# Kernel tuning notes

Measured on AMD Instinct MI355X. Metric: run time of the kernel, lower is better.

Reference implementation:

```python
import jax, jax.numpy as jnp
import numpy as np

S = 4096            # num tokens (single causal sequence)
HID = 1024          # hidden_size
NH = 16             # num query heads
NKV = 4             # num kv heads
HD = 64             # head_dim
THETA = 10000.0
Q_SIZE = NH * HD
KV_SIZE = NKV * HD


def setup_inputs() -> dict:
    key = jax.random.key(0)
    k1, k2, k3 = jax.random.split(key, 3)
    return {
        "positions": jnp.arange(S, dtype=jnp.int32),
        "hidden_states": jax.random.normal(k1, (S, 2 * HID), dtype=jnp.float32),
        "w_qkv": jax.random.normal(k2, (Q_SIZE + 2 * KV_SIZE, 2 * HID), dtype=jnp.float32) * 0.02,
        "w_o": jax.random.normal(k3, (HID, Q_SIZE), dtype=jnp.float32) * 0.02,
    }


def _rope(x, positions):
    # x: [S, H, HD]; neox-style rotate-half RoPE
    half = HD // 2
    inv_freq = 1.0 / (THETA ** (jnp.arange(0, half, dtype=jnp.float32) / half))
    freqs = positions.astype(jnp.float32)[:, None] * inv_freq  # [S, half]
    cos = jnp.cos(freqs)[:, None, :]  # [S, 1, half]
    sin = jnp.sin(freqs)[:, None, :]
    x1, x2 = x[..., :half], x[..., half:]
    return jnp.concatenate([x1 * cos - x2 * sin, x2 * cos + x1 * sin], axis=-1)


def reference(positions, hidden_states, w_qkv, w_o):
    qkv = hidden_states @ w_qkv.T  # [S, Q_SIZE + 2*KV_SIZE]
    q = qkv[:, :Q_SIZE].reshape(S, NH, HD)
    k = qkv[:, Q_SIZE:Q_SIZE + KV_SIZE].reshape(S, NKV, HD)
    v = qkv[:, Q_SIZE + KV_SIZE:].reshape(S, NKV, HD)
    q = _rope(q, positions)
    k = _rope(k, positions)
    # GQA: group query heads over kv heads
    g = NH // NKV
    qg = q.reshape(S, NKV, g, HD)
    scale = HD ** -0.5
    scores = jnp.einsum("qhgd,thd->hgqt", qg, k) * scale  # [NKV, g, S, S]
    causal = positions[:, None] >= positions[None, :]      # [S, S]
    scores = jnp.where(causal[None, None], scores, jnp.finfo(scores.dtype).min)
    probs = jax.nn.softmax(scores, axis=-1)
    o = jnp.einsum("hgqt,thd->qhgd", probs, v).reshape(S, Q_SIZE)
    return o @ w_o.T  # [S, HID]
```

## Files before the change

### kernel.cpp

```cpp
#include <hip/hip_runtime.h>
#include <math.h>

#define S_LEN   4096
#define NHEADS  16
#define NKVH    4
#define HDIM    64
#define QKV_N   1536
#define HID2    2048
#define OUT_N   1024

typedef __attribute__((ext_vector_type(8))) __bf16 bf16x8;
typedef __attribute__((ext_vector_type(4))) __bf16 bf16x4;
typedef __attribute__((ext_vector_type(4))) float  f32x4;

#define GL_LDS16(gaddr, laddr)                                                  \
  __builtin_amdgcn_global_load_lds(                                             \
      (const __attribute__((address_space(1))) unsigned int*)(gaddr),           \
      (__attribute__((address_space(3))) unsigned int*)(laddr), 16, 0, 0)

__global__ __launch_bounds__(256) void cvt_all(const float* __restrict__ hid,
                                               const float* __restrict__ wq,
                                               const float* __restrict__ wo,
                                               __bf16* __restrict__ hid_bf,
                                               __bf16* __restrict__ wq_bf,
                                               __bf16* __restrict__ wo_bf) {
  const int n1 = S_LEN * HID2;
  const int n2 = QKV_N * HID2;
  int i = (blockIdx.x * blockDim.x + threadIdx.x) * 8;
  const float* src; __bf16* dst; int off;
  if (i < n1)           { src = hid; dst = hid_bf; off = i; }
  else if (i < n1 + n2) { src = wq;  dst = wq_bf;  off = i - n1; }
  else                  { src = wo;  dst = wo_bf;  off = i - n1 - n2; }
  float4 a = *(const float4*)(src + off);
  float4 b = *(const float4*)(src + off + 4);
  bf16x8 o = {(__bf16)a.x,(__bf16)a.y,(__bf16)a.z,(__bf16)a.w,
              (__bf16)b.x,(__bf16)b.y,(__bf16)b.z,(__bf16)b.w};
  *(bf16x8*)(dst + off) = o;
}

__global__ __launch_bounds__(256) void rope_table(const int* __restrict__ positions,
                                                  float* __restrict__ ct,
                                                  float* __restrict__ st) {
  int i = blockIdx.x * blockDim.x + threadIdx.x;
  int s = i >> 5, d = i & 31;
  double inv = pow(10000.0, -(double)d / 32.0);
  double fr = (double)positions[s] * inv;
  ct[i] = (float)cos(fr);
  st[i] = (float)sin(fr);
}

template<int BM, bool C_BF16>
__global__ __launch_bounds__(256) void gemm_m97(const __bf16* __restrict__ A,
                                                const __bf16* __restrict__ B,
                                                void* __restrict__ Cp,
                                                int M, int N, int K) {
  constexpr int TM = BM / 32;
  __shared__ __align__(16) __bf16 As[BM * 32];
  __shared__ __align__(16) __bf16 Bs[128 * 32];
  const int tid  = threadIdx.x;
  const int bm   = blockIdx.x, bn = blockIdx.y;
  const int wave = tid >> 6, lane = tid & 63;
  const int quad = lane >> 4, col = lane & 15;
  const int wm = (wave >> 1) * (BM / 2), wn = (wave & 1) * 64;

  const int lrow = lane >> 2, lcol = (lane & 3) * 8;
  const __bf16* Ag = A + (size_t)(bm * BM + wave * (BM / 4) + lrow) * K + lcol;
  const __bf16* Bg = B + (size_t)(bn * 128 + wave * 32 + lrow) * K + lcol;
  __bf16* AsW = As + wave * (BM / 4) * 32;
  __bf16* BsW = Bs + wave * 32 * 32;

  f32x4 acc[TM][4];
#pragma unroll
  for (int i = 0; i < TM; ++i)
#pragma unroll
    for (int j = 0; j < 4; ++j) acc[i][j] = (f32x4){0.f, 0.f, 0.f, 0.f};

  for (int kk = 0; kk < K; kk += 32) {
    __syncthreads();
#pragma unroll
    for (int u = 0; u < BM / 64; ++u)
      GL_LDS16(Ag + kk + (size_t)(u * 16) * K, AsW + u * 16 * 32);
    GL_LDS16(Bg + kk,                  BsW);
    GL_LDS16(Bg + kk + (size_t)16 * K, BsW + 16 * 32);
    __syncthreads();

    bf16x8 a[TM], b[4];
#pragma unroll
    for (int tm = 0; tm < TM; ++tm)
      a[tm] = *(const bf16x8*)&As[(wm + tm * 16 + col) * 32 + quad * 8];
#pragma unroll
    for (int tn = 0; tn < 4; ++tn)
      b[tn] = *(const bf16x8*)&Bs[(wn + tn * 16 + col) * 32 + quad * 8];
#pragma unroll
    for (int tm = 0; tm < TM; ++tm)
#pragma unroll
      for (int tn = 0; tn < 4; ++tn)
        acc[tm][tn] = __builtin_amdgcn_mfma_f32_16x16x32_bf16(a[tm], b[tn], acc[tm][tn], 0, 0, 0);
  }

#pragma unroll
  for (int tm = 0; tm < TM; ++tm)
#pragma unroll
    for (int tn = 0; tn < 4; ++tn) {
      int row = bm * BM + wm + tm * 16 + quad * 4;
      int cg  = bn * 128 + wn + tn * 16 + col;
#pragma unroll
      for (int r = 0; r < 4; ++r) {
        if constexpr (C_BF16)
          ((__bf16*)Cp)[(size_t)(row + r) * N + cg] = (__bf16)acc[tm][tn][r];
        else
          ((float*)Cp)[(size_t)(row + r) * N + cg] = acc[tm][tn][r];
      }
    }
}

__global__ __launch_bounds__(256) void rope_cast(const __bf16* __restrict__ qkv,
                                                 const float* __restrict__ ct,
                                                 const float* __restrict__ st,
                                                 __bf16* __restrict__ qb,
                                                 __bf16* __restrict__ kb) {
  int g = blockIdx.x * blockDim.x + threadIdx.x;
  int d = g & 31;
  int rem = g >> 5;
  int head = rem % 20;
  int s = rem / 20;
  bool isq = head < NHEADS;
  const __bf16* src = qkv + (size_t)s * QKV_N + (isq ? head * 64 : 1024 + (head - 16) * 64);
  float c  = ct[s * 32 + d];
  float sn = st[s * 32 + d];
  float x1 = (float)src[d], x2 = (float)src[d + 32];
  float y1 = x1 * c - x2 * sn;
  float y2 = x2 * c + x1 * sn;
  float scl = isq ? 0.125f : 1.0f;
  __bf16* dst = isq ? (qb + (size_t)s * 1024 + head * 64)
                    : (kb + (size_t)s * 256 + (head - 16) * 64);
  dst[d]      = (__bf16)(y1 * scl);
  dst[d + 32] = (__bf16)(y2 * scl);
}

__global__ __launch_bounds__(256) void v_transpose(const __bf16* __restrict__ qkv,
                                                   __bf16* __restrict__ vT) {
  __shared__ __align__(16) __bf16 Ts[64][72];
  const int sb = blockIdx.x, kvh = blockIdx.y, t = threadIdx.x;
  const int r = t >> 2, c16 = (t & 3) * 16;
  const __bf16* src = qkv + (size_t)(sb * 64 + r) * QKV_N + 1280 + kvh * 64 + c16;
  bf16x8 v0 = *(const bf16x8*)src;
  bf16x8 v1 = *(const bf16x8*)(src + 8);
#pragma unroll
  for (int u = 0; u < 8; ++u) {
    Ts[c16 + u][r]     = v0[u];
    Ts[c16 + 8 + u][r] = v1[u];
  }
  __syncthreads();
  __bf16* dst = vT + ((size_t)kvh * 64 + r) * S_LEN + sb * 64 + c16;
  *(bf16x8*)dst       = *(const bf16x8*)&Ts[r][c16];
  *(bf16x8*)(dst + 8) = *(const bf16x8*)&Ts[r][c16 + 8];
}

__global__ __launch_bounds__(256) void attn_mfma2(const __bf16* __restrict__ qg,
                                                  const __bf16* __restrict__ kg,
                                                  const __bf16* __restrict__ vg,
                                                  __bf16* __restrict__ ob) {
  __shared__ __align__(16) __bf16 lds[26624];
  __bf16* Qs = lds;
  __bf16* Ks = lds + 8192;
  __bf16* Vs = lds + 17408;

  const int tid = threadIdx.x;
  const int h = blockIdx.x;
  const int yy = blockIdx.y;
  const int qb = (yy < 16) ? yy : 47 - yy;
  const int kvh = h >> 2;
  const int wave = tid >> 6, lane = tid & 63;
  const int quad = lane >> 4, col = lane & 15;
  const int quad4 = quad * 4;
  const int qbase = qb * 128 + wave * 32;
  const int ntiles = 2 * qb + 2;

  {
    const int r = tid >> 1, c = (tid & 1) * 32;
    const __bf16* src = qg + (size_t)(qb * 128 + r) * 1024 + h * 64 + c;
    *(bf16x8*)&Qs[r * 64 + c]      = *(const bf16x8*)(src);
    *(bf16x8*)&Qs[r * 64 + c + 8]  = *(const bf16x8*)(src + 8);
    *(bf16x8*)&Qs[r * 64 + c + 16] = *(const bf16x8*)(src + 16);
    *(bf16x8*)&Qs[r * 64 + c + 24] = *(const bf16x8*)(src + 24);
  }

  const int sr = tid >> 2, sc = (tid & 3) * 16;
  const __bf16* kptr = kg + (size_t)sr * 256 + kvh * 64 + sc;
  const __bf16* vptr = vg + ((size_t)kvh * 64 + sr) * S_LEN + sc;
  bf16x8 kr0 = *(const bf16x8*)(kptr);
  bf16x8 kr1 = *(const bf16x8*)(kptr + 8);
  bf16x8 vr0 = *(const bf16x8*)(vptr);
  bf16x8 vr1 = *(const bf16x8*)(vptr + 8);

  __syncthreads();

  bf16x8 qf[2][2];
#pragma unroll
  for (int nq = 0; nq < 2; ++nq)
#pragma unroll
    for (int ks = 0; ks < 2; ++ks)
      qf[nq][ks] = *(const bf16x8*)&Qs[(wave * 32 + nq * 16 + col) * 64 + ks * 32 + quad * 8];

  __bf16* Pw = Qs + wave * 2048;

  f32x4 o[2][4];
  float lacc[2] = {0.f, 0.f};
#pragma unroll
  for (int i = 0; i < 2; ++i)
#pragma unroll
    for (int j = 0; j < 4; ++j) o[i][j] = (f32x4){0.f, 0.f, 0.f, 0.f};

  for (int kt = 0; kt < ntiles; ++kt) {
    const int cur = kt & 1;
    {
      __bf16* kd = Ks + cur * 4608 + sr * 72 + sc;
      *(bf16x8*)kd       = kr0;
      *(bf16x8*)(kd + 8) = kr1;
      __bf16* vd = Vs + cur * 4608 + sr * 72 + sc;
      *(bf16x8*)vd       = vr0;
      *(bf16x8*)(vd + 8) = vr1;
    }
    if (kt + 1 < ntiles) {
      const __bf16* kn = kptr + (size_t)(kt + 1) * 64 * 256;
      const __bf16* vn = vptr + (size_t)(kt + 1) * 64;
      kr0 = *(const bf16x8*)(kn);
      kr1 = *(const bf16x8*)(kn + 8);
      vr0 = *(const bf16x8*)(vn);
      vr1 = *(const bf16x8*)(vn + 8);
    }
    __syncthreads();

    if (kt * 64 > qbase + 31) continue;

    f32x4 sf[4][2];
#pragma unroll
    for (int mt = 0; mt < 4; ++mt)
#pragma unroll
      for (int nq = 0; nq < 2; ++nq) sf[mt][nq] = (f32x4){0.f, 0.f, 0.f, 0.f};
#pragma unroll
    for (int ks = 0; ks < 2; ++ks) {
      bf16x8 kf[4];
#pragma unroll
      for (int mt = 0; mt < 4; ++mt)
        kf[mt] = *(const bf16x8*)&Ks[cur * 4608 + (mt * 16 + col) * 72 + ks * 32 + quad * 8];
#pragma unroll
      for (int mt = 0; mt < 4; ++mt)
#pragma unroll
        for (int nq = 0; nq < 2; ++nq)
          sf[mt][nq] = __builtin_amdgcn_mfma_f32_16x16x32_bf16(kf[mt], qf[nq][ks], sf[mt][nq], 0, 0, 0);
    }

    const bool full = (kt * 64 + 63 <= qbase);
#pragma unroll
    for (int mt = 0; mt < 4; ++mt) {
      const int tb = mt * 16 + quad4;
#pragma unroll
      for (int nq = 0; nq < 2; ++nq) {
        const int thr = qbase + nq * 16 + col - kt * 64;
        float p0 = __expf(sf[mt][nq][0]);
        float p1 = __expf(sf[mt][nq][1]);
        float p2 = __expf(sf[mt][nq][2]);
        float p3 = __expf(sf[mt][nq][3]);
        if (!full) {
          if (tb + 0 > thr) p0 = 0.f;
          if (tb + 1 > thr) p1 = 0.f;
          if (tb + 2 > thr) p2 = 0.f;
          if (tb + 3 > thr) p3 = 0.f;
        }
        lacc[nq] += (p0 + p1) + (p2 + p3);
        const int g = ((mt * 2 + (quad >> 1)) ^ (col & 7));
        bf16x4 pk = {(__bf16)p0, (__bf16)p1, (__bf16)p2, (__bf16)p3};
        *(bf16x4*)&Pw[(nq * 16 + col) * 64 + g * 8 + (quad & 1) * 4] = pk;
      }
    }

#pragma unroll
    for (int ks = 0; ks < 2; ++ks) {
      bf16x8 pf[2], vf[4];
#pragma unroll
      for (int mq = 0; mq < 2; ++mq)
        pf[mq] = *(const bf16x8*)&Pw[(mq * 16 + col) * 64 + (((ks * 4 + quad) ^ (col & 7)) * 8)];
#pragma unroll
      for (int nd = 0; nd < 4; ++nd)
        vf[nd] = *(const bf16x8*)&Vs[cur * 4608 + (nd * 16 + col) * 72 + ks * 32 + quad * 8];
#pragma unroll
      for (int mq = 0; mq < 2; ++mq)
#pragma unroll
        for (int nd = 0; nd < 4; ++nd)
          o[mq][nd] = __builtin_amdgcn_mfma_f32_16x16x32_bf16(pf[mq], vf[nd], o[mq][nd], 0, 0, 0);
    }
  }

#pragma unroll
  for (int nq = 0; nq < 2; ++nq) {
    lacc[nq] += __shfl_xor(lacc[nq], 16, 64);
    lacc[nq] += __shfl_xor(lacc[nq], 32, 64);
  }
  __syncthreads();
  float* lsh = (float*)Pw;
  if (lane < 16) { lsh[lane] = lacc[0]; lsh[16 + lane] = lacc[1]; }
  __syncthreads();

#pragma unroll
  for (int mq = 0; mq < 2; ++mq)
#pragma unroll
    for (int r = 0; r < 4; ++r) {
      float linv = 1.f / lsh[mq * 16 + quad4 + r];
      int row = qb * 128 + wave * 32 + mq * 16 + quad4 + r;
#pragma unroll
      for (int nd = 0; nd < 4; ++nd)
        ob[(size_t)row * 1024 + h * 64 + nd * 16 + col] = (__bf16)(o[mq][nd][r] * linv);
    }
}

extern "C" void kernel_launch(void* const* d_in, const int* in_sizes, int n_in,
                              void* d_out, int out_size, void* d_ws, size_t ws_size,
                              hipStream_t stream) {
  const int*   positions = (const int*)d_in[0];
  const float* hidden    = (const float*)d_in[1];
  const float* w_qkv     = (const float*)d_in[2];
  const float* w_o       = (const float*)d_in[3];
  float* out = (float*)d_out;

  char* ws = (char*)d_ws;
  __bf16* qkv_bf  = (__bf16*)ws;
  __bf16* attn_bf = (__bf16*)ws;
  __bf16* hid_bf  = (__bf16*)(ws + 12582912);
  __bf16* q_bf    = (__bf16*)(ws + 12582912);
  __bf16* k_bf    = (__bf16*)(ws + 20971520);
  __bf16* vT      = (__bf16*)(ws + 23068672);
  float*  ct      = (float*)(ws + 29360128);
  float*  st      = (float*)(ws + 29884416);
  __bf16* wq_bf   = (__bf16*)(ws + 30408704);
  __bf16* wo_bf   = (__bf16*)(ws + 36700160);

  cvt_all<<<(S_LEN * HID2 + QKV_N * HID2 + OUT_N * OUT_N) / 8 / 256, 256, 0, stream>>>(
      hidden, w_qkv, w_o, hid_bf, wq_bf, wo_bf);
  rope_table<<<S_LEN * 32 / 256, 256, 0, stream>>>(positions, ct, st);

  gemm_m97<64, true><<<dim3(S_LEN / 64, QKV_N / 128), 256, 0, stream>>>(
      hid_bf, wq_bf, qkv_bf, S_LEN, QKV_N, HID2);

  rope_cast<<<(S_LEN * 20 * 32) / 256, 256, 0, stream>>>(qkv_bf, ct, st, q_bf, k_bf);
  v_transpose<<<dim3(S_LEN / 64, NKVH), 256, 0, stream>>>(qkv_bf, vT);

  attn_mfma2<<<dim3(NHEADS, 32), 256, 0, stream>>>(q_bf, k_bf, vT, attn_bf);

  gemm_m97<64, false><<<dim3(S_LEN / 64, OUT_N / 128), 256, 0, stream>>>(
      attn_bf, wo_bf, out, S_LEN, OUT_N, OUT_N);
}
```

Before: 257.0 us.

## Split attention KV range in two per query block and combine partials

Each query block's causal KV range is split into two equal halves, each handled by its own workgroup. This doubles the attention grid to improve occupancy and load balance across CUs. Each half writes a normalized bf16 partial output and its softmax denominator. A new elementwise kernel blends the two partials, weighting each by its denominator. The cost is an extra launch, extra partial-output traffic to workspace, and bf16 rounding of the intermediate partials; the workspace layout is reshuffled to fit them.

```diff
diff --git a/kernel.cpp b/kernel.cpp
--- a/kernel.cpp
+++ b/kernel.cpp
@@ -157,10 +157,12 @@
   *(bf16x8*)(dst + 8) = *(const bf16x8*)&Ts[r][c16 + 8];
 }
 
-__global__ __launch_bounds__(256) void attn_mfma2(const __bf16* __restrict__ qg,
+__global__ __launch_bounds__(256) void attn_split(const __bf16* __restrict__ qg,
                                                   const __bf16* __restrict__ kg,
                                                   const __bf16* __restrict__ vg,
-                                                  __bf16* __restrict__ ob) {
+                                                  __bf16* __restrict__ op0,
+                                                  __bf16* __restrict__ op1,
+                                                  float* __restrict__ lp) {
   __shared__ __align__(16) __bf16 lds[26624];
   __bf16* Qs = lds;
   __bf16* Ks = lds + 8192;
@@ -169,13 +171,15 @@
   const int tid = threadIdx.x;
   const int h = blockIdx.x;
   const int yy = blockIdx.y;
-  const int qb = (yy < 16) ? yy : 47 - yy;
+  const int qq = yy >> 1, split = yy & 1;
+  const int qb = (qq < 16) ? qq : 47 - qq;
   const int kvh = h >> 2;
   const int wave = tid >> 6, lane = tid & 63;
   const int quad = lane >> 4, col = lane & 15;
   const int quad4 = quad * 4;
   const int qbase = qb * 128 + wave * 32;
-  const int ntiles = 2 * qb + 2;
+  const int kt0 = split * (qb + 1);
+  const int ktEnd = kt0 + qb + 1;
 
   {
     const int r = tid >> 1, c = (tid & 1) * 32;
@@ -189,10 +193,10 @@
   const int sr = tid >> 2, sc = (tid & 3) * 16;
   const __bf16* kptr = kg + (size_t)sr * 256 + kvh * 64 + sc;
   const __bf16* vptr = vg + ((size_t)kvh * 64 + sr) * S_LEN + sc;
-  bf16x8 kr0 = *(const bf16x8*)(kptr);
-  bf16x8 kr1 = *(const bf16x8*)(kptr + 8);
-  bf16x8 vr0 = *(const bf16x8*)(vptr);
-  bf16x8 vr1 = *(const bf16x8*)(vptr + 8);
+  bf16x8 kr0 = *(const bf16x8*)(kptr + (size_t)kt0 * 64 * 256);
+  bf16x8 kr1 = *(const bf16x8*)(kptr + (size_t)kt0 * 64 * 256 + 8);
+  bf16x8 vr0 = *(const bf16x8*)(vptr + (size_t)kt0 * 64);
+  bf16x8 vr1 = *(const bf16x8*)(vptr + (size_t)kt0 * 64 + 8);
 
   __syncthreads();
 
@@ -212,8 +216,8 @@
 #pragma unroll
     for (int j = 0; j < 4; ++j) o[i][j] = (f32x4){0.f, 0.f, 0.f, 0.f};
 
-  for (int kt = 0; kt < ntiles; ++kt) {
-    const int cur = kt & 1;
+  for (int kt = kt0; kt < ktEnd; ++kt) {
+    const int cur = (kt - kt0) & 1;
     {
       __bf16* kd = Ks + cur * 4608 + sr * 72 + sc;
       *(bf16x8*)kd       = kr0;
@@ -222,7 +226,7 @@
       *(bf16x8*)vd       = vr0;
       *(bf16x8*)(vd + 8) = vr1;
     }
-    if (kt + 1 < ntiles) {
+    if (kt + 1 < ktEnd) {
       const __bf16* kn = kptr + (size_t)(kt + 1) * 64 * 256;
       const __bf16* vn = vptr + (size_t)(kt + 1) * 64;
       kr0 = *(const bf16x8*)(kn);
@@ -303,16 +307,47 @@
   if (lane < 16) { lsh[lane] = lacc[0]; lsh[16 + lane] = lacc[1]; }
   __syncthreads();
 
+  __bf16* op = split ? op1 : op0;
 #pragma unroll
   for (int mq = 0; mq < 2; ++mq)
 #pragma unroll
     for (int r = 0; r < 4; ++r) {
-      float linv = 1.f / lsh[mq * 16 + quad4 + r];
+      float l = lsh[mq * 16 + quad4 + r];
+      float linv = (l > 0.f) ? 1.f / l : 0.f;
       int row = qb * 128 + wave * 32 + mq * 16 + quad4 + r;
 #pragma unroll
       for (int nd = 0; nd < 4; ++nd)
-        ob[(size_t)row * 1024 + h * 64 + nd * 16 + col] = (__bf16)(o[mq][nd][r] * linv);
-    }
+        op[(size_t)row * 1024 + h * 64 + nd * 16 + col] =
+            (__bf16)(o[mq][nd][r] * linv);
+    }
+  if (col == 0) {
+#pragma unroll
+    for (int mq = 0; mq < 2; ++mq)
+#pragma unroll
+      for (int r = 0; r < 4; ++r)
+        lp[(size_t)(split * S_LEN + qb * 128 + wave * 32 + mq * 16 + quad4 + r) * NHEADS + h] =
+            lsh[mq * 16 + quad4 + r];
+  }
+}
+
+__global__ __launch_bounds__(256) void attn_combine(const __bf16* __restrict__ op0,
+                                                    const __bf16* __restrict__ op1,
+                                                    const float* __restrict__ lp,
+                                                    __bf16* __restrict__ ob) {
+  int i = blockIdx.x * 256 + threadIdx.x;
+  int row = i >> 7, c8 = (i & 127) * 8;
+  int h = c8 >> 6;
+  float l0 = lp[(size_t)row * NHEADS + h];
+  float l1 = lp[(size_t)(S_LEN + row) * NHEADS + h];
+  float inv = 1.f / (l0 + l1);
+  float w0 = l0 * inv, w1 = l1 * inv;
+  bf16x8 a = *(const bf16x8*)(op0 + (size_t)row * 1024 + c8);
+  bf16x8 b = *(const bf16x8*)(op1 + (size_t)row * 1024 + c8);
+  bf16x8 o;
+#pragma unroll
+  for (int u = 0; u < 8; ++u)
+    o[u] = (__bf16)((float)a[u] * w0 + (float)b[u] * w1);
+  *(bf16x8*)(ob + (size_t)row * 1024 + c8) = o;
 }
 
 extern "C" void kernel_launch(void* const* d_in, const int* in_sizes, int n_in,
@@ -326,6 +361,7 @@
 
   char* ws = (char*)d_ws;
   __bf16* qkv_bf  = (__bf16*)ws;
+  __bf16* Opart0  = (__bf16*)ws;
   __bf16* attn_bf = (__bf16*)ws;
   __bf16* hid_bf  = (__bf16*)(ws + 12582912);
   __bf16* q_bf    = (__bf16*)(ws + 12582912);
@@ -333,8 +369,10 @@
   __bf16* vT      = (__bf16*)(ws + 23068672);
   float*  ct      = (float*)(ws + 29360128);
   float*  st      = (float*)(ws + 29884416);
+  float*  lpart   = (float*)(ws + 29360128);
   __bf16* wq_bf   = (__bf16*)(ws + 30408704);
-  __bf16* wo_bf   = (__bf16*)(ws + 36700160);
+  __bf16* Opart1  = (__bf16*)(ws + 30408704);
+  __bf16* wo_bf   = (__bf16*)(ws + 38797312);
 
   cvt_all<<<(S_LEN * HID2 + QKV_N * HID2 + OUT_N * OUT_N) / 8 / 256, 256, 0, stream>>>(
       hidden, w_qkv, w_o, hid_bf, wq_bf, wo_bf);
@@ -346,7 +384,8 @@
   rope_cast<<<(S_LEN * 20 * 32) / 256, 256, 0, stream>>>(qkv_bf, ct, st, q_bf, k_bf);
   v_transpose<<<dim3(S_LEN / 64, NKVH), 256, 0, stream>>>(qkv_bf, vT);
 
-  attn_mfma2<<<dim3(NHEADS, 32), 256, 0, stream>>>(q_bf, k_bf, vT, attn_bf);
+  attn_split<<<dim3(NHEADS, 64), 256, 0, stream>>>(q_bf, k_bf, vT, Opart0, Opart1, lpart);
+  attn_combine<<<S_LEN * 128 / 256, 256, 0, stream>>>(Opart0, Opart1, lpart, attn_bf);
 
   gemm_m97<64, false><<<dim3(S_LEN / 64, OUT_N / 128), 256, 0, stream>>>(
       attn_bf, wo_bf, out, S_LEN, OUT_N, OUT_N);
```

Result: faster. 239.0 us (-7.0%).
